# Optimization experiments

Hardware: AMD Instinct MI355X
Metric: run time of the kernel (lower is better)

Reference implementation:

```python
import jax, jax.numpy as jnp
import numpy as np

B, S, D = 1, 2048, 1024
NH, NKV, HD = 16, 4, 64
N_REP = NH // NKV


def _rope_tables(seq_len, half_dim, base=10000.0):
    inv_freq = 1.0 / (base ** (np.arange(0, half_dim, dtype=np.float32) / half_dim))
    t = np.arange(seq_len, dtype=np.float32)
    freqs = np.outer(t, inv_freq)  # (S, HD//2)
    return jnp.asarray(np.cos(freqs)), jnp.asarray(np.sin(freqs))


def setup_inputs() -> dict:
    key = jax.random.key(0)
    ks = jax.random.split(key, 5)
    x = jax.random.normal(ks[0], (B, S, D), dtype=jnp.float32)
    rope_cos, rope_sin = _rope_tables(S, HD // 2)
    sd = 1.0 / np.sqrt(D)
    Wq = jax.random.normal(ks[1], (D, NH * HD), dtype=jnp.float32) * sd
    Wk = jax.random.normal(ks[2], (D, NKV * HD), dtype=jnp.float32) * sd
    Wv = jax.random.normal(ks[3], (D, NKV * HD), dtype=jnp.float32) * sd
    Wo = jax.random.normal(ks[4], (NH * HD, D), dtype=jnp.float32) * sd
    return {"x": x, "rope_cos": rope_cos, "rope_sin": rope_sin,
            "Wq": Wq, "Wk": Wk, "Wv": Wv, "Wo": Wo}


def _apply_rope(t, cos, sin):
    # t: (B, H, S, HD); cos/sin: (S, HD//2). Rotate-half convention.
    t1, t2 = jnp.split(t, 2, axis=-1)
    c = cos[None, None, :, :]
    s = sin[None, None, :, :]
    return jnp.concatenate([t1 * c - t2 * s, t2 * c + t1 * s], axis=-1)


def reference(x, rope_cos, rope_sin, Wq, Wk, Wv, Wo):
    b, s, _ = x.shape
    # projections -> (B, H, S, HD)
    q = (x @ Wq).reshape(b, s, NH, HD).transpose(0, 2, 1, 3)
    k = (x @ Wk).reshape(b, s, NKV, HD).transpose(0, 2, 1, 3)
    v = (x @ Wv).reshape(b, s, NKV, HD).transpose(0, 2, 1, 3)
    q = _apply_rope(q, rope_cos, rope_sin)
    k = _apply_rope(k, rope_cos, rope_sin)
    # GQA expansion (repeat_interleave on head axis)
    k = jnp.repeat(k, N_REP, axis=1)
    v = jnp.repeat(v, N_REP, axis=1)
    scale = HD ** -0.5
    scores = jnp.einsum('bhqd,bhkd->bhqk', q, k) * scale
    causal = jnp.tril(jnp.ones((s, s), dtype=bool))
    scores = jnp.where(causal[None, None], scores, jnp.float32(-jnp.inf))
    attn = jax.nn.softmax(scores, axis=-1)
    out = jnp.einsum('bhqk,bhkd->bhqd', attn, v)  # (B, H, S, HD)
    out = out.transpose(0, 2, 1, 3).reshape(b, s, NH * HD)
    return out @ Wo
```

## Files before the change

kernel.cpp:

```cpp
#include <hip/hip_runtime.h>

typedef unsigned short ushort_t;
typedef __attribute__((ext_vector_type(8))) short short8;
typedef __attribute__((ext_vector_type(4))) float f32x4;
typedef __attribute__((ext_vector_type(4))) unsigned short ushort4v;
typedef __attribute__((ext_vector_type(8))) unsigned short ushort8v;

#define S_LEN 2048
#define D_MODEL 1024
#define NH 16
#define NKV 4
#define HD 64

__device__ __forceinline__ ushort_t f2bf(float f) {
    unsigned u = __float_as_uint(f);
    u += 0x7fffu + ((u >> 16) & 1u);
    return (ushort_t)(u >> 16);
}

__device__ __forceinline__ void cp16(void* lds, const void* g) {
    __builtin_amdgcn_global_load_lds(
        (__attribute__((address_space(1))) void*)g,
        (__attribute__((address_space(3))) void*)lds, 16, 0, 0);
}

__global__ __launch_bounds__(256) void prep_kernel(
    const float* __restrict__ x, ushort_t* __restrict__ xb,
    const float* __restrict__ Wq, const float* __restrict__ Wk,
    const float* __restrict__ Wv, const float* __restrict__ Wo,
    ushort_t* __restrict__ WqT, ushort_t* __restrict__ WkT,
    ushort_t* __restrict__ WvT, ushort_t* __restrict__ WoT)
{
    const int t = threadIdx.x;
    if (blockIdx.z == 4) {
        const int b  = blockIdx.y * 16 + blockIdx.x;
        const int i0 = (b * 256 + t) * 4;
        #pragma unroll
        for (int rep = 0; rep < 8; ++rep) {
            const int i = i0 + rep * 262144;
            float4 v = *(const float4*)(x + i);
            ushort4v o = { f2bf(v.x), f2bf(v.y), f2bf(v.z), f2bf(v.w) };
            *(ushort4v*)(xb + i) = o;
        }
        return;
    }
    __shared__ ushort_t T[64 * 72];
    const float* W; ushort_t* WT; int N;
    switch (blockIdx.z) {
        case 0:  W = Wq; WT = WqT; N = 1024; break;
        case 1:  W = Wk; WT = WkT; N = 256;  break;
        case 2:  W = Wv; WT = WvT; N = 256;  break;
        default: W = Wo; WT = WoT; N = 1024; break;
    }
    const int n0 = blockIdx.y * 64;
    if (n0 >= N) return;
    const int k0 = blockIdx.x * 64;
    const int kr = t >> 4, nc = (t & 15) * 4;
    #pragma unroll
    for (int p = 0; p < 4; ++p) {
        const int k = kr + p * 16;
        float4 v = *(const float4*)(W + (size_t)(k0 + k) * N + n0 + nc);
        T[(nc + 0) * 72 + k] = f2bf(v.x);
        T[(nc + 1) * 72 + k] = f2bf(v.y);
        T[(nc + 2) * 72 + k] = f2bf(v.z);
        T[(nc + 3) * 72 + k] = f2bf(v.w);
    }
    __syncthreads();
    const int n = t >> 2, seg = (t & 3) * 16;
    ushort8v a = *(ushort8v*)&T[n * 72 + seg];
    ushort8v b = *(ushort8v*)&T[n * 72 + seg + 8];
    *(ushort8v*)(WT + (size_t)(n0 + n) * 1024 + k0 + seg)     = a;
    *(ushort8v*)(WT + (size_t)(n0 + n) * 1024 + k0 + seg + 8) = b;
}

__global__ __launch_bounds__(256, 2) void gemm_qkv_mfma(
    const ushort_t* __restrict__ xb, const ushort_t* __restrict__ WqT,
    const ushort_t* __restrict__ WkT, const ushort_t* __restrict__ WvT,
    const float* __restrict__ rc, const float* __restrict__ rs,
    ushort_t* __restrict__ Qb, ushort_t* __restrict__ Kb,
    ushort_t* __restrict__ Vtb)
{
    __shared__ ushort_t As[4][64 * 64];
    __shared__ ushort_t Bs[4][64 * 64];

    const int t = threadIdx.x;
    const int lane = t & 63, wave = t >> 6;
    const int wr = wave >> 1, wc = wave & 1;
    const int quad = lane >> 4, l15 = lane & 15;
    const int lq = lane >> 3, lr = lane & 7;
    const int swz_st = (lr ^ lq) * 8;
    const int l7 = l15 & 7;
    const int fsw0 = (quad ^ l7) * 8;
    const int fsw1 = ((quad + 4) ^ l7) * 8;

    const int m0 = blockIdx.x * 64;
    const int cy = blockIdx.y;

    const ushort_t* WT; int nloc;
    if (cy < 16)      { WT = WqT; nloc = cy * 64; }
    else if (cy < 20) { WT = WkT; nloc = (cy - 16) * 64; }
    else              { WT = WvT; nloc = (cy - 20) * 64; }

    f32x4 acc[2][2];
    #pragma unroll
    for (int i = 0; i < 2; ++i)
        #pragma unroll
        for (int j = 0; j < 2; ++j) acc[i][j] = (f32x4)0.f;

    auto stage = [&](int buf, int k0) {
        #pragma unroll
        for (int i = 0; i < 2; ++i) {
            const int r = wave * 16 + i * 8 + lq;
            cp16(&As[buf][(wave * 16 + i * 8) * 64],
                 xb + (size_t)(m0 + r) * 1024 + k0 + swz_st);
            cp16(&Bs[buf][(wave * 16 + i * 8) * 64],
                 WT + (size_t)(nloc + r) * 1024 + k0 + swz_st);
        }
    };

    auto compute = [&](int cur) {
        const ushort_t* Ac = &As[cur][0];
        const ushort_t* Bc = &Bs[cur][0];
        #pragma unroll
        for (int h = 0; h < 2; ++h) {
            const int fsw = h ? fsw1 : fsw0;
            short8 av[2], bv[2];
            #pragma unroll
            for (int i = 0; i < 2; ++i)
                av[i] = *(const short8*)&Ac[(wr * 32 + i * 16 + l15) * 64 + fsw];
            #pragma unroll
            for (int j = 0; j < 2; ++j)
                bv[j] = *(const short8*)&Bc[(wc * 16 + j * 32 + l15) * 64 + fsw];
            #pragma unroll
            for (int i = 0; i < 2; ++i)
                #pragma unroll
                for (int j = 0; j < 2; ++j)
                    acc[i][j] = __builtin_amdgcn_mfma_f32_16x16x32_bf16(
                        av[i], bv[j], acc[i][j], 0, 0, 0);
        }
    };

    stage(0, 0);
    stage(1, 64);
    stage(2, 128);

    for (int kk = 0; kk < 14; ++kk) {
        asm volatile("s_waitcnt vmcnt(8)" ::: "memory");
        __builtin_amdgcn_s_barrier();
        __builtin_amdgcn_sched_barrier(0);
        if (kk < 13) stage((kk + 3) & 3, (kk + 3) * 64);
        compute(kk & 3);
    }
    asm volatile("s_waitcnt vmcnt(4)" ::: "memory");
    __builtin_amdgcn_s_barrier();
    __builtin_amdgcn_sched_barrier(0);
    compute(2);
    asm volatile("s_waitcnt vmcnt(0)" ::: "memory");
    __builtin_amdgcn_s_barrier();
    __builtin_amdgcn_sched_barrier(0);
    compute(3);

    if (cy < 20) {
        ushort_t* dst = (cy < 16) ? Qb : Kb;
        const int h = (cy < 16) ? cy : (cy - 16);
        const int d = wc * 16 + l15;
        #pragma unroll
        for (int i = 0; i < 2; ++i) {
            #pragma unroll
            for (int reg = 0; reg < 4; ++reg) {
                const int s = m0 + wr * 32 + i * 16 + quad * 4 + reg;
                const float c  = rc[s * 32 + d];
                const float sn = rs[s * 32 + d];
                const float v1 = acc[i][0][reg];
                const float v2 = acc[i][1][reg];
                dst[((size_t)h * S_LEN + s) * HD + d]      = f2bf(v1 * c - v2 * sn);
                dst[((size_t)h * S_LEN + s) * HD + d + 32] = f2bf(v2 * c + v1 * sn);
            }
        }
    } else {
        const int vh = cy - 20;
        #pragma unroll
        for (int i = 0; i < 2; ++i) {
            const int s0 = m0 + wr * 32 + i * 16 + quad * 4;
            #pragma unroll
            for (int j = 0; j < 2; ++j) {
                const int d = wc * 16 + j * 32 + l15;
                ushort4v o = { f2bf(acc[i][j][0]), f2bf(acc[i][j][1]),
                               f2bf(acc[i][j][2]), f2bf(acc[i][j][3]) };
                *(ushort4v*)&Vtb[((size_t)vh * HD + d) * S_LEN + s0] = o;
            }
        }
    }
}

__global__ __launch_bounds__(256, 2) void attn_mfma(
    const ushort_t* __restrict__ Qb, const ushort_t* __restrict__ Kb,
    const ushort_t* __restrict__ Vtb, ushort_t* __restrict__ attnb)
{
    __shared__ ushort_t Ks[2][2][64 * 64];
    __shared__ ushort_t Vs[2][2][64 * 64];
    __shared__ ushort_t Ps[4][16 * 72];

    const int t = threadIdx.x;
    const int lane = t & 63, wave = t >> 6;
    const int quad = lane >> 4, l15 = lane & 15;
    const int lq = lane >> 3, lr = lane & 7;
    const int swz_st = (lr ^ lq) * 8;
    const int l7 = l15 & 7;
    const int fsw0 = (quad ^ l7) * 8;
    const int fsw1 = ((quad + 4) ^ l7) * 8;

    const int h  = blockIdx.x;
    const int y  = blockIdx.y;
    const int qt = (y < 16) ? y : 47 - y;
    const int q0 = qt * 64;
    const int kvh = h >> 2;
    const int qrow0 = q0 + wave * 16;

    const ushort_t* Qg = Qb + ((size_t)h * S_LEN + qrow0) * HD;
    const ushort_t* Kg = Kb + (size_t)kvh * S_LEN * HD;
    const ushort_t* Vg = Vtb + (size_t)kvh * HD * S_LEN;

    short8 aq0 = *(const short8*)(Qg + (size_t)l15 * HD + quad * 8);
    short8 aq1 = *(const short8*)(Qg + (size_t)l15 * HD + 32 + quad * 8);

    float ps4[4] = {0.f, 0.f, 0.f, 0.f};
    f32x4 Oacc[4];
    #pragma unroll
    for (int jb = 0; jb < 4; ++jb) Oacc[jb] = (f32x4)0.f;

    const int nround = (qt + 2) >> 1;

    auto stage = [&](int buf, int kvbase) {
        #pragma unroll
        for (int u = 0; u < 2; ++u)
            #pragma unroll
            for (int i = 0; i < 2; ++i) {
                const int r = wave * 16 + i * 8 + lq;
                cp16(&Ks[buf][u][(wave * 16 + i * 8) * 64],
                     Kg + (size_t)(kvbase + u * 64 + r) * 64 + swz_st);
                cp16(&Vs[buf][u][(wave * 16 + i * 8) * 64],
                     Vg + (size_t)r * 2048 + kvbase + u * 64 + swz_st);
            }
    };

    stage(0, 0);
    __syncthreads();

    ushort_t* Pw = &Ps[wave][0];

    for (int round = 0; round < nround; ++round) {
        const int cur = round & 1;
        if (round + 1 < nround) stage(cur ^ 1, (round + 1) * 128);

        #pragma unroll
        for (int u = 0; u < 2; ++u) {
            const int kv0 = round * 128 + u * 64;
            if (kv0 > q0 + 63) break;
            const ushort_t* Kc = &Ks[cur][u][0];
            const ushort_t* Vc = &Vs[cur][u][0];

            f32x4 sv[4];
            #pragma unroll
            for (int jb = 0; jb < 4; ++jb) {
                short8 b0 = *(const short8*)&Kc[(jb * 16 + l15) * 64 + fsw0];
                short8 b1 = *(const short8*)&Kc[(jb * 16 + l15) * 64 + fsw1];
                f32x4 z = (f32x4)0.f;
                z = __builtin_amdgcn_mfma_f32_16x16x32_bf16(aq0, b0, z, 0, 0, 0);
                z = __builtin_amdgcn_mfma_f32_16x16x32_bf16(aq1, b1, z, 0, 0, 0);
                sv[jb] = z;
            }

            const bool diag = (kv0 == q0);
            #pragma unroll
            for (int jb = 0; jb < 4; ++jb) {
                const int col = kv0 + jb * 16 + l15;
                #pragma unroll
                for (int reg = 0; reg < 4; ++reg) {
                    float e = __expf(sv[jb][reg] * 0.125f);
                    if (diag && col > qrow0 + quad * 4 + reg) e = 0.f;
                    sv[jb][reg] = e;
                    ps4[reg] += e;
                }
            }

            #pragma unroll
            for (int jb = 0; jb < 4; ++jb)
                #pragma unroll
                for (int reg = 0; reg < 4; ++reg)
                    Pw[(quad * 4 + reg) * 72 + jb * 16 + l15] = f2bf(sv[jb][reg]);
            short8 p0 = *(const short8*)&Pw[l15 * 72 + quad * 8];
            short8 p1 = *(const short8*)&Pw[l15 * 72 + 32 + quad * 8];

            #pragma unroll
            for (int jb = 0; jb < 4; ++jb) {
                short8 v0 = *(const short8*)&Vc[(jb * 16 + l15) * 64 + fsw0];
                short8 v1 = *(const short8*)&Vc[(jb * 16 + l15) * 64 + fsw1];
                Oacc[jb] = __builtin_amdgcn_mfma_f32_16x16x32_bf16(p0, v0, Oacc[jb], 0, 0, 0);
                Oacc[jb] = __builtin_amdgcn_mfma_f32_16x16x32_bf16(p1, v1, Oacc[jb], 0, 0, 0);
            }
        }

        __syncthreads();
    }

    #pragma unroll
    for (int reg = 0; reg < 4; ++reg) {
        float l = ps4[reg];
        l += __shfl_xor(l, 1);
        l += __shfl_xor(l, 2);
        l += __shfl_xor(l, 4);
        l += __shfl_xor(l, 8);
        const float inv = 1.f / l;
        const int s = qrow0 + quad * 4 + reg;
        #pragma unroll
        for (int jb = 0; jb < 4; ++jb)
            attnb[(size_t)s * D_MODEL + h * HD + jb * 16 + l15] =
                f2bf(Oacc[jb][reg] * inv);
    }
}

__global__ __launch_bounds__(256, 2) void gemm_out_mfma(
    const ushort_t* __restrict__ Ab, const ushort_t* __restrict__ WoT,
    float* __restrict__ out)
{
    __shared__ ushort_t As[4][64 * 64];
    __shared__ ushort_t Bs[4][64 * 64];

    const int t = threadIdx.x;
    const int lane = t & 63, wave = t >> 6;
    const int wr = wave >> 1, wc = wave & 1;
    const int quad = lane >> 4, l15 = lane & 15;
    const int lq = lane >> 3, lr = lane & 7;
    const int swz_st = (lr ^ lq) * 8;
    const int l7 = l15 & 7;
    const int fsw0 = (quad ^ l7) * 8;
    const int fsw1 = ((quad + 4) ^ l7) * 8;

    const int m0 = blockIdx.x * 64;
    const int n0 = blockIdx.y * 64;

    f32x4 acc[2][2];
    #pragma unroll
    for (int i = 0; i < 2; ++i)
        #pragma unroll
        for (int j = 0; j < 2; ++j) acc[i][j] = (f32x4)0.f;

    auto stage = [&](int buf, int k0) {
        #pragma unroll
        for (int i = 0; i < 2; ++i) {
            const int r = wave * 16 + i * 8 + lq;
            cp16(&As[buf][(wave * 16 + i * 8) * 64],
                 Ab + (size_t)(m0 + r) * 1024 + k0 + swz_st);
            cp16(&Bs[buf][(wave * 16 + i * 8) * 64],
                 WoT + (size_t)(n0 + r) * 1024 + k0 + swz_st);
        }
    };

    auto compute = [&](int cur) {
        const ushort_t* Ac = &As[cur][0];
        const ushort_t* Bc = &Bs[cur][0];
        #pragma unroll
        for (int h = 0; h < 2; ++h) {
            const int fsw = h ? fsw1 : fsw0;
            short8 av[2], bv[2];
            #pragma unroll
            for (int i = 0; i < 2; ++i)
                av[i] = *(const short8*)&Ac[(wr * 32 + i * 16 + l15) * 64 + fsw];
            #pragma unroll
            for (int j = 0; j < 2; ++j)
                bv[j] = *(const short8*)&Bc[(wc * 32 + j * 16 + l15) * 64 + fsw];
            #pragma unroll
            for (int i = 0; i < 2; ++i)
                #pragma unroll
                for (int j = 0; j < 2; ++j)
                    acc[i][j] = __builtin_amdgcn_mfma_f32_16x16x32_bf16(
                        av[i], bv[j], acc[i][j], 0, 0, 0);
        }
    };

    stage(0, 0);
    stage(1, 64);
    stage(2, 128);

    for (int kk = 0; kk < 14; ++kk) {
        asm volatile("s_waitcnt vmcnt(8)" ::: "memory");
        __builtin_amdgcn_s_barrier();
        __builtin_amdgcn_sched_barrier(0);
        if (kk < 13) stage((kk + 3) & 3, (kk + 3) * 64);
        compute(kk & 3);
    }
    asm volatile("s_waitcnt vmcnt(4)" ::: "memory");
    __builtin_amdgcn_s_barrier();
    __builtin_amdgcn_sched_barrier(0);
    compute(2);
    asm volatile("s_waitcnt vmcnt(0)" ::: "memory");
    __builtin_amdgcn_s_barrier();
    __builtin_amdgcn_sched_barrier(0);
    compute(3);

    #pragma unroll
    for (int i = 0; i < 2; ++i)
        #pragma unroll
        for (int reg = 0; reg < 4; ++reg) {
            const int s = m0 + wr * 32 + i * 16 + quad * 4 + reg;
            #pragma unroll
            for (int j = 0; j < 2; ++j)
                out[(size_t)s * D_MODEL + n0 + wc * 32 + j * 16 + l15] = acc[i][j][reg];
        }
}

extern "C" void kernel_launch(void* const* d_in, const int* in_sizes, int n_in,
                              void* d_out, int out_size, void* d_ws, size_t ws_size,
                              hipStream_t stream)
{
    const float* x  = (const float*)d_in[0];
    const float* rc = (const float*)d_in[1];
    const float* rs = (const float*)d_in[2];
    const float* Wq = (const float*)d_in[3];
    const float* Wk = (const float*)d_in[4];
    const float* Wv = (const float*)d_in[5];
    const float* Wo = (const float*)d_in[6];
    float* out = (float*)d_out;

    ushort_t* xb   = (ushort_t*)d_ws;
    ushort_t* WqT  = xb   + (size_t)2048 * 1024;
    ushort_t* WkT  = WqT  + (size_t)1024 * 1024;
    ushort_t* WvT  = WkT  + (size_t)256 * 1024;
    ushort_t* WoT  = WvT  + (size_t)256 * 1024;
    ushort_t* Qb   = WoT  + (size_t)1024 * 1024;
    ushort_t* Kb   = Qb   + (size_t)NH * S_LEN * HD;
    ushort_t* Vtb  = Kb   + (size_t)NKV * S_LEN * HD;
    ushort_t* attnb= Vtb  + (size_t)NKV * HD * S_LEN;

    prep_kernel<<<dim3(16, 16, 5), 256, 0, stream>>>(x, xb, Wq, Wk, Wv, Wo,
                                                     WqT, WkT, WvT, WoT);
    gemm_qkv_mfma<<<dim3(32, 24), 256, 0, stream>>>(xb, WqT, WkT, WvT,
                                                    rc, rs, Qb, Kb, Vtb);
    attn_mfma<<<dim3(NH, 32), 256, 0, stream>>>(Qb, Kb, Vtb, attnb);
    gemm_out_mfma<<<dim3(32, 16), 256, 0, stream>>>(attnb, WoT, out);
}
```

Before: 140.5 us.

## Replace double-buffered 128-key rounds with 4-slot 64-key prefetch pipeline in attention

The attention kernel used to stage K/V in 128-key rounds with double buffering and a full __syncthreads per round. It now stages 64-key tiles into a 4-slot ring, prefetching three tiles ahead. Each step waits with explicit s_waitcnt vmcnt counts before a raw s_barrier. The aim is to hide global-to-LDS latency better and avoid loading a wasted half-round past the diagonal. The hand-written vmcnt counts must match the number of outstanding loads exactly, and there is still one barrier per 64-key tile.

```diff
diff --git a/kernel.cpp b/kernel.cpp
--- a/kernel.cpp
+++ b/kernel.cpp
@@ -197,8 +197,8 @@
     const ushort_t* __restrict__ Qb, const ushort_t* __restrict__ Kb,
     const ushort_t* __restrict__ Vtb, ushort_t* __restrict__ attnb)
 {
-    __shared__ ushort_t Ks[2][2][64 * 64];
-    __shared__ ushort_t Vs[2][2][64 * 64];
+    __shared__ ushort_t Ks[4][64 * 64];
+    __shared__ ushort_t Vs[4][64 * 64];
     __shared__ ushort_t Ps[4][16 * 72];
 
     const int t = threadIdx.x;
@@ -229,79 +229,79 @@
     #pragma unroll
     for (int jb = 0; jb < 4; ++jb) Oacc[jb] = (f32x4)0.f;
 
-    const int nround = (qt + 2) >> 1;
-
-    auto stage = [&](int buf, int kvbase) {
-        #pragma unroll
-        for (int u = 0; u < 2; ++u)
-            #pragma unroll
-            for (int i = 0; i < 2; ++i) {
-                const int r = wave * 16 + i * 8 + lq;
-                cp16(&Ks[buf][u][(wave * 16 + i * 8) * 64],
-                     Kg + (size_t)(kvbase + u * 64 + r) * 64 + swz_st);
-                cp16(&Vs[buf][u][(wave * 16 + i * 8) * 64],
-                     Vg + (size_t)r * 2048 + kvbase + u * 64 + swz_st);
+    const int nsub = qt + 1;
+
+    auto stage64 = [&](int s) {
+        const int kv0 = s * 64;
+        ushort_t* Kd = &Ks[s & 3][0];
+        ushort_t* Vd = &Vs[s & 3][0];
+        #pragma unroll
+        for (int i = 0; i < 2; ++i) {
+            const int rr = wave * 16 + i * 8;
+            const int r = rr + lq;
+            cp16(&Kd[rr * 64], Kg + (size_t)(kv0 + r) * 64 + swz_st);
+            cp16(&Vd[rr * 64], Vg + (size_t)r * 2048 + kv0 + swz_st);
+        }
+    };
+
+    stage64(0);
+    if (nsub > 1) stage64(1);
+    if (nsub > 2) stage64(2);
+
+    ushort_t* Pw = &Ps[wave][0];
+
+    for (int s = 0; s < nsub; ++s) {
+        const int rem = nsub - 1 - s;
+        if (rem >= 2)      asm volatile("s_waitcnt vmcnt(8)" ::: "memory");
+        else if (rem == 1) asm volatile("s_waitcnt vmcnt(4)" ::: "memory");
+        else               asm volatile("s_waitcnt vmcnt(0)" ::: "memory");
+        __builtin_amdgcn_s_barrier();
+        __builtin_amdgcn_sched_barrier(0);
+        if (s + 3 < nsub) stage64(s + 3);
+
+        const int kv0 = s * 64;
+        const ushort_t* Kc = &Ks[s & 3][0];
+        const ushort_t* Vc = &Vs[s & 3][0];
+
+        f32x4 sv[4];
+        #pragma unroll
+        for (int jb = 0; jb < 4; ++jb) {
+            short8 b0 = *(const short8*)&Kc[(jb * 16 + l15) * 64 + fsw0];
+            short8 b1 = *(const short8*)&Kc[(jb * 16 + l15) * 64 + fsw1];
+            f32x4 z = (f32x4)0.f;
+            z = __builtin_amdgcn_mfma_f32_16x16x32_bf16(aq0, b0, z, 0, 0, 0);
+            z = __builtin_amdgcn_mfma_f32_16x16x32_bf16(aq1, b1, z, 0, 0, 0);
+            sv[jb] = z;
+        }
+
+        const bool diag = (kv0 == q0);
+        #pragma unroll
+        for (int jb = 0; jb < 4; ++jb) {
+            const int col = kv0 + jb * 16 + l15;
+            #pragma unroll
+            for (int reg = 0; reg < 4; ++reg) {
+                float e = __expf(sv[jb][reg] * 0.125f);
+                if (diag && col > qrow0 + quad * 4 + reg) e = 0.f;
+                sv[jb][reg] = e;
+                ps4[reg] += e;
             }
-    };
-
-    stage(0, 0);
-    __syncthreads();
-
-    ushort_t* Pw = &Ps[wave][0];
-
-    for (int round = 0; round < nround; ++round) {
-        const int cur = round & 1;
-        if (round + 1 < nround) stage(cur ^ 1, (round + 1) * 128);
-
-        #pragma unroll
-        for (int u = 0; u < 2; ++u) {
-            const int kv0 = round * 128 + u * 64;
-            if (kv0 > q0 + 63) break;
-            const ushort_t* Kc = &Ks[cur][u][0];
-            const ushort_t* Vc = &Vs[cur][u][0];
-
-            f32x4 sv[4];
-            #pragma unroll
-            for (int jb = 0; jb < 4; ++jb) {
-                short8 b0 = *(const short8*)&Kc[(jb * 16 + l15) * 64 + fsw0];
-                short8 b1 = *(const short8*)&Kc[(jb * 16 + l15) * 64 + fsw1];
-                f32x4 z = (f32x4)0.f;
-                z = __builtin_amdgcn_mfma_f32_16x16x32_bf16(aq0, b0, z, 0, 0, 0);
-                z = __builtin_amdgcn_mfma_f32_16x16x32_bf16(aq1, b1, z, 0, 0, 0);
-                sv[jb] = z;
-            }
-
-            const bool diag = (kv0 == q0);
-            #pragma unroll
-            for (int jb = 0; jb < 4; ++jb) {
-                const int col = kv0 + jb * 16 + l15;
-                #pragma unroll
-                for (int reg = 0; reg < 4; ++reg) {
-                    float e = __expf(sv[jb][reg] * 0.125f);
-                    if (diag && col > qrow0 + quad * 4 + reg) e = 0.f;
-                    sv[jb][reg] = e;
-                    ps4[reg] += e;
-                }
-            }
-
-            #pragma unroll
-            for (int jb = 0; jb < 4; ++jb)
-                #pragma unroll
-                for (int reg = 0; reg < 4; ++reg)
-                    Pw[(quad * 4 + reg) * 72 + jb * 16 + l15] = f2bf(sv[jb][reg]);
-            short8 p0 = *(const short8*)&Pw[l15 * 72 + quad * 8];
-            short8 p1 = *(const short8*)&Pw[l15 * 72 + 32 + quad * 8];
-
-            #pragma unroll
-            for (int jb = 0; jb < 4; ++jb) {
-                short8 v0 = *(const short8*)&Vc[(jb * 16 + l15) * 64 + fsw0];
-                short8 v1 = *(const short8*)&Vc[(jb * 16 + l15) * 64 + fsw1];
-                Oacc[jb] = __builtin_amdgcn_mfma_f32_16x16x32_bf16(p0, v0, Oacc[jb], 0, 0, 0);
-                Oacc[jb] = __builtin_amdgcn_mfma_f32_16x16x32_bf16(p1, v1, Oacc[jb], 0, 0, 0);
-            }
-        }
-
-        __syncthreads();
+        }
+
+        #pragma unroll
+        for (int jb = 0; jb < 4; ++jb)
+            #pragma unroll
+            for (int reg = 0; reg < 4; ++reg)
+                Pw[(quad * 4 + reg) * 72 + jb * 16 + l15] = f2bf(sv[jb][reg]);
+        short8 p0 = *(const short8*)&Pw[l15 * 72 + quad * 8];
+        short8 p1 = *(const short8*)&Pw[l15 * 72 + 32 + quad * 8];
+
+        #pragma unroll
+        for (int jb = 0; jb < 4; ++jb) {
+            short8 v0 = *(const short8*)&Vc[(jb * 16 + l15) * 64 + fsw0];
+            short8 v1 = *(const short8*)&Vc[(jb * 16 + l15) * 64 + fsw1];
+            Oacc[jb] = __builtin_amdgcn_mfma_f32_16x16x32_bf16(p0, v0, Oacc[jb], 0, 0, 0);
+            Oacc[jb] = __builtin_amdgcn_mfma_f32_16x16x32_bf16(p1, v1, Oacc[jb], 0, 0, 0);
+        }
     }
 
     #pragma unroll
```

Result: slower. 146.3 us (+4.1%).

## Split attention tile into 2x2 wave grid over query and KV halves

Applied to the files above, without the earlier changes.

Each wave now covers 32 query rows and half of each 64-key chunk, not 16 rows over all keys. K and V fragments loaded from LDS are reused across two query sub-tiles, which halves LDS fragment reads per MFMA. Waves whose KV half lies fully above the diagonal skip that chunk. The two KV-half partial outputs and row sums are combined through LDS at the end, which adds an extra barrier and a reduction step.

```diff
diff --git a/kernel.cpp b/kernel.cpp
--- a/kernel.cpp
+++ b/kernel.cpp
@@ -199,7 +199,7 @@
 {
     __shared__ ushort_t Ks[2][2][64 * 64];
     __shared__ ushort_t Vs[2][2][64 * 64];
-    __shared__ ushort_t Ps[4][16 * 72];
+    __shared__ ushort_t Ps[4][32 * 40];
 
     const int t = threadIdx.x;
     const int lane = t & 63, wave = t >> 6;
@@ -207,27 +207,44 @@
     const int lq = lane >> 3, lr = lane & 7;
     const int swz_st = (lr ^ lq) * 8;
     const int l7 = l15 & 7;
-    const int fsw0 = (quad ^ l7) * 8;
-    const int fsw1 = ((quad + 4) ^ l7) * 8;
+
+    const int qh  = wave >> 1;
+    const int kvh = wave & 1;
+    const int kvL0 = kvh * 32;
+
+    const int fswK0 = (quad ^ l7) * 8;
+    const int fswK1 = ((quad + 4) ^ l7) * 8;
+    const int fswV  = (((kvh << 2) + quad) ^ l7) * 8;
 
     const int h  = blockIdx.x;
     const int y  = blockIdx.y;
     const int qt = (y < 16) ? y : 47 - y;
     const int q0 = qt * 64;
-    const int kvh = h >> 2;
-    const int qrow0 = q0 + wave * 16;
+    const int kvhead = h >> 2;
+    const int qrow0 = q0 + qh * 32;
 
     const ushort_t* Qg = Qb + ((size_t)h * S_LEN + qrow0) * HD;
-    const ushort_t* Kg = Kb + (size_t)kvh * S_LEN * HD;
-    const ushort_t* Vg = Vtb + (size_t)kvh * HD * S_LEN;
-
-    short8 aq0 = *(const short8*)(Qg + (size_t)l15 * HD + quad * 8);
-    short8 aq1 = *(const short8*)(Qg + (size_t)l15 * HD + 32 + quad * 8);
-
-    float ps4[4] = {0.f, 0.f, 0.f, 0.f};
-    f32x4 Oacc[4];
-    #pragma unroll
-    for (int jb = 0; jb < 4; ++jb) Oacc[jb] = (f32x4)0.f;
+    const ushort_t* Kg = Kb + (size_t)kvhead * S_LEN * HD;
+    const ushort_t* Vg = Vtb + (size_t)kvhead * HD * S_LEN;
+
+    short8 aq[2][2];
+    #pragma unroll
+    for (int mq = 0; mq < 2; ++mq)
+        #pragma unroll
+        for (int kh = 0; kh < 2; ++kh)
+            aq[mq][kh] = *(const short8*)(Qg + (size_t)(mq * 16 + l15) * HD
+                                          + kh * 32 + quad * 8);
+
+    float ps[2][4];
+    #pragma unroll
+    for (int mq = 0; mq < 2; ++mq)
+        #pragma unroll
+        for (int r = 0; r < 4; ++r) ps[mq][r] = 0.f;
+    f32x4 Oacc[2][4];
+    #pragma unroll
+    for (int mq = 0; mq < 2; ++mq)
+        #pragma unroll
+        for (int jb = 0; jb < 4; ++jb) Oacc[mq][jb] = (f32x4)0.f;
 
     const int nround = (qt + 2) >> 1;
 
@@ -257,66 +274,112 @@
         for (int u = 0; u < 2; ++u) {
             const int kv0 = round * 128 + u * 64;
             if (kv0 > q0 + 63) break;
+            const bool diag = (kv0 == q0);
+            if (diag && kvL0 > qh * 32 + 31) continue;
             const ushort_t* Kc = &Ks[cur][u][0];
             const ushort_t* Vc = &Vs[cur][u][0];
 
-            f32x4 sv[4];
+            short8 kb[2][2];
+            #pragma unroll
+            for (int jbl = 0; jbl < 2; ++jbl) {
+                kb[jbl][0] = *(const short8*)&Kc[(kvL0 + jbl * 16 + l15) * 64 + fswK0];
+                kb[jbl][1] = *(const short8*)&Kc[(kvL0 + jbl * 16 + l15) * 64 + fswK1];
+            }
+
+            f32x4 sv[2][2];
+            #pragma unroll
+            for (int mq = 0; mq < 2; ++mq)
+                #pragma unroll
+                for (int jbl = 0; jbl < 2; ++jbl) {
+                    f32x4 z = (f32x4)0.f;
+                    z = __builtin_amdgcn_mfma_f32_16x16x32_bf16(aq[mq][0], kb[jbl][0], z, 0, 0, 0);
+                    z = __builtin_amdgcn_mfma_f32_16x16x32_bf16(aq[mq][1], kb[jbl][1], z, 0, 0, 0);
+                    sv[mq][jbl] = z;
+                }
+
+            #pragma unroll
+            for (int mq = 0; mq < 2; ++mq)
+                #pragma unroll
+                for (int jbl = 0; jbl < 2; ++jbl) {
+                    const int colg = kv0 + kvL0 + jbl * 16 + l15;
+                    #pragma unroll
+                    for (int reg = 0; reg < 4; ++reg) {
+                        float e = __expf(sv[mq][jbl][reg] * 0.125f);
+                        const int qg = qrow0 + mq * 16 + quad * 4 + reg;
+                        if (diag && colg > qg) e = 0.f;
+                        sv[mq][jbl][reg] = e;
+                        ps[mq][reg] += e;
+                    }
+                }
+
+            #pragma unroll
+            for (int mq = 0; mq < 2; ++mq)
+                #pragma unroll
+                for (int jbl = 0; jbl < 2; ++jbl)
+                    #pragma unroll
+                    for (int reg = 0; reg < 4; ++reg)
+                        Pw[(mq * 16 + quad * 4 + reg) * 40 + jbl * 16 + l15] =
+                            f2bf(sv[mq][jbl][reg]);
+            short8 pa[2];
+            #pragma unroll
+            for (int mq = 0; mq < 2; ++mq)
+                pa[mq] = *(const short8*)&Pw[(mq * 16 + l15) * 40 + quad * 8];
+
             #pragma unroll
             for (int jb = 0; jb < 4; ++jb) {
-                short8 b0 = *(const short8*)&Kc[(jb * 16 + l15) * 64 + fsw0];
-                short8 b1 = *(const short8*)&Kc[(jb * 16 + l15) * 64 + fsw1];
-                f32x4 z = (f32x4)0.f;
-                z = __builtin_amdgcn_mfma_f32_16x16x32_bf16(aq0, b0, z, 0, 0, 0);
-                z = __builtin_amdgcn_mfma_f32_16x16x32_bf16(aq1, b1, z, 0, 0, 0);
-                sv[jb] = z;
-            }
-
-            const bool diag = (kv0 == q0);
-            #pragma unroll
-            for (int jb = 0; jb < 4; ++jb) {
-                const int col = kv0 + jb * 16 + l15;
-                #pragma unroll
-                for (int reg = 0; reg < 4; ++reg) {
-                    float e = __expf(sv[jb][reg] * 0.125f);
-                    if (diag && col > qrow0 + quad * 4 + reg) e = 0.f;
-                    sv[jb][reg] = e;
-                    ps4[reg] += e;
+                short8 vb = *(const short8*)&Vc[(jb * 16 + l15) * 64 + fswV];
+                Oacc[0][jb] = __builtin_amdgcn_mfma_f32_16x16x32_bf16(pa[0], vb, Oacc[0][jb], 0, 0, 0);
+                Oacc[1][jb] = __builtin_amdgcn_mfma_f32_16x16x32_bf16(pa[1], vb, Oacc[1][jb], 0, 0, 0);
+            }
+        }
+
+        __syncthreads();
+    }
+
+    #pragma unroll
+    for (int mq = 0; mq < 2; ++mq)
+        #pragma unroll
+        for (int reg = 0; reg < 4; ++reg) {
+            float l = ps[mq][reg];
+            l += __shfl_xor(l, 1);
+            l += __shfl_xor(l, 2);
+            l += __shfl_xor(l, 4);
+            l += __shfl_xor(l, 8);
+            ps[mq][reg] = l;
+        }
+
+    float* Rbuf = (float*)&Ks[0][0][0];
+    if (kvh == 1) {
+        #pragma unroll
+        for (int mq = 0; mq < 2; ++mq)
+            #pragma unroll
+            for (int reg = 0; reg < 4; ++reg) {
+                const int row = mq * 16 + quad * 4 + reg;
+                #pragma unroll
+                for (int jb = 0; jb < 4; ++jb)
+                    Rbuf[qh * 2176 + row * 68 + jb * 16 + l15] = Oacc[mq][jb][reg];
+                if (l15 == 0)
+                    Rbuf[qh * 2176 + row * 68 + 64] = ps[mq][reg];
+            }
+    }
+    __syncthreads();
+    if (kvh == 0) {
+        #pragma unroll
+        for (int mq = 0; mq < 2; ++mq)
+            #pragma unroll
+            for (int reg = 0; reg < 4; ++reg) {
+                const int row = mq * 16 + quad * 4 + reg;
+                const float ltot = ps[mq][reg] + Rbuf[qh * 2176 + row * 68 + 64];
+                const float inv = 1.f / ltot;
+                const int sq = qrow0 + row;
+                #pragma unroll
+                for (int jb = 0; jb < 4; ++jb) {
+                    const float o = Oacc[mq][jb][reg]
+                                  + Rbuf[qh * 2176 + row * 68 + jb * 16 + l15];
+                    attnb[(size_t)sq * D_MODEL + h * HD + jb * 16 + l15] =
+                        f2bf(o * inv);
                 }
             }
-
-            #pragma unroll
-            for (int jb = 0; jb < 4; ++jb)
-                #pragma unroll
-                for (int reg = 0; reg < 4; ++reg)
-                    Pw[(quad * 4 + reg) * 72 + jb * 16 + l15] = f2bf(sv[jb][reg]);
-            short8 p0 = *(const short8*)&Pw[l15 * 72 + quad * 8];
-            short8 p1 = *(const short8*)&Pw[l15 * 72 + 32 + quad * 8];
-
-            #pragma unroll
-            for (int jb = 0; jb < 4; ++jb) {
-                short8 v0 = *(const short8*)&Vc[(jb * 16 + l15) * 64 + fsw0];
-                short8 v1 = *(const short8*)&Vc[(jb * 16 + l15) * 64 + fsw1];
-                Oacc[jb] = __builtin_amdgcn_mfma_f32_16x16x32_bf16(p0, v0, Oacc[jb], 0, 0, 0);
-                Oacc[jb] = __builtin_amdgcn_mfma_f32_16x16x32_bf16(p1, v1, Oacc[jb], 0, 0, 0);
-            }
-        }
-
-        __syncthreads();
-    }
-
-    #pragma unroll
-    for (int reg = 0; reg < 4; ++reg) {
-        float l = ps4[reg];
-        l += __shfl_xor(l, 1);
-        l += __shfl_xor(l, 2);
-        l += __shfl_xor(l, 4);
-        l += __shfl_xor(l, 8);
-        const float inv = 1.f / l;
-        const int s = qrow0 + quad * 4 + reg;
-        #pragma unroll
-        for (int jb = 0; jb < 4; ++jb)
-            attnb[(size_t)s * D_MODEL + h * HD + jb * 16 + l15] =
-                f2bf(Oacc[jb][reg] * inv);
     }
 }
 
```

Measured after the change: 140.7 us. About the same (+0.1%).

## Halve attention query tile to 32 rows with 2-wave blocks and more blocks

Applied to the files above, without the earlier changes.

The attention kernel now uses 128-thread blocks, each covering 32 query rows, and launches twice as many blocks, with a new balanced tile-ordering map. The K/V staging no longer double-buffers: each round loads two 64-key subtiles, synchronises, then computes. The smaller tiles waste less work on the causal diagonal and give finer load balancing. In exchange, each K/V tile is reloaded by more blocks, and global loads no longer overlap with compute.

```diff
diff --git a/kernel.cpp b/kernel.cpp
--- a/kernel.cpp
+++ b/kernel.cpp
@@ -193,13 +193,13 @@
     }
 }
 
-__global__ __launch_bounds__(256, 2) void attn_mfma(
+__global__ __launch_bounds__(128, 2) void attn_mfma(
     const ushort_t* __restrict__ Qb, const ushort_t* __restrict__ Kb,
     const ushort_t* __restrict__ Vtb, ushort_t* __restrict__ attnb)
 {
-    __shared__ ushort_t Ks[2][2][64 * 64];
-    __shared__ ushort_t Vs[2][2][64 * 64];
-    __shared__ ushort_t Ps[4][16 * 72];
+    __shared__ ushort_t Ks[2][64 * 64];
+    __shared__ ushort_t Vs[2][64 * 64];
+    __shared__ ushort_t Ps[2][16 * 72];
 
     const int t = threadIdx.x;
     const int lane = t & 63, wave = t >> 6;
@@ -210,10 +210,10 @@
     const int fsw0 = (quad ^ l7) * 8;
     const int fsw1 = ((quad + 4) ^ l7) * 8;
 
-    const int h  = blockIdx.x;
-    const int y  = blockIdx.y;
-    const int qt = (y < 16) ? y : 47 - y;
-    const int q0 = qt * 64;
+    const int h = blockIdx.x;
+    const int z = blockIdx.y;
+    const int T = (z & 16) ? ((z < 32) ? 47 - z : 111 - z) : z;
+    const int q0 = T * 32;
     const int kvh = h >> 2;
     const int qrow0 = q0 + wave * 16;
 
@@ -229,49 +229,49 @@
     #pragma unroll
     for (int jb = 0; jb < 4; ++jb) Oacc[jb] = (f32x4)0.f;
 
-    const int nround = (qt + 2) >> 1;
-
-    auto stage = [&](int buf, int kvbase) {
-        #pragma unroll
-        for (int u = 0; u < 2; ++u)
-            #pragma unroll
-            for (int i = 0; i < 2; ++i) {
-                const int r = wave * 16 + i * 8 + lq;
-                cp16(&Ks[buf][u][(wave * 16 + i * 8) * 64],
-                     Kg + (size_t)(kvbase + u * 64 + r) * 64 + swz_st);
-                cp16(&Vs[buf][u][(wave * 16 + i * 8) * 64],
-                     Vg + (size_t)r * 2048 + kvbase + u * 64 + swz_st);
-            }
+    const int nsub = (q0 + 31) / 64 + 1;
+    const int nround = (nsub + 1) >> 1;
+
+    auto stage = [&](int u, int sidx) {
+        const int kv0 = sidx * 64;
+        #pragma unroll
+        for (int i = 0; i < 4; ++i) {
+            const int rr = wave * 32 + i * 8;
+            const int r = rr + lq;
+            cp16(&Ks[u][rr * 64], Kg + (size_t)(kv0 + r) * 64 + swz_st);
+            cp16(&Vs[u][rr * 64], Vg + (size_t)r * 2048 + kv0 + swz_st);
+        }
     };
 
-    stage(0, 0);
-    __syncthreads();
-
     ushort_t* Pw = &Ps[wave][0];
 
     for (int round = 0; round < nround; ++round) {
-        const int cur = round & 1;
-        if (round + 1 < nround) stage(cur ^ 1, (round + 1) * 128);
+        const int s0 = round * 2;
+        if (round) __syncthreads();
+        stage(0, s0);
+        if (s0 + 1 < nsub) stage(1, s0 + 1);
+        __syncthreads();
 
         #pragma unroll
         for (int u = 0; u < 2; ++u) {
-            const int kv0 = round * 128 + u * 64;
-            if (kv0 > q0 + 63) break;
-            const ushort_t* Kc = &Ks[cur][u][0];
-            const ushort_t* Vc = &Vs[cur][u][0];
+            const int sidx = s0 + u;
+            if (sidx >= nsub) break;
+            const int kv0 = sidx * 64;
+            const bool diag = (sidx == nsub - 1);
+            const ushort_t* Kc = &Ks[u][0];
+            const ushort_t* Vc = &Vs[u][0];
 
             f32x4 sv[4];
             #pragma unroll
             for (int jb = 0; jb < 4; ++jb) {
                 short8 b0 = *(const short8*)&Kc[(jb * 16 + l15) * 64 + fsw0];
                 short8 b1 = *(const short8*)&Kc[(jb * 16 + l15) * 64 + fsw1];
-                f32x4 z = (f32x4)0.f;
-                z = __builtin_amdgcn_mfma_f32_16x16x32_bf16(aq0, b0, z, 0, 0, 0);
-                z = __builtin_amdgcn_mfma_f32_16x16x32_bf16(aq1, b1, z, 0, 0, 0);
-                sv[jb] = z;
+                f32x4 zv = (f32x4)0.f;
+                zv = __builtin_amdgcn_mfma_f32_16x16x32_bf16(aq0, b0, zv, 0, 0, 0);
+                zv = __builtin_amdgcn_mfma_f32_16x16x32_bf16(aq1, b1, zv, 0, 0, 0);
+                sv[jb] = zv;
             }
 
-            const bool diag = (kv0 == q0);
             #pragma unroll
             for (int jb = 0; jb < 4; ++jb) {
                 const int col = kv0 + jb * 16 + l15;
@@ -300,8 +300,6 @@
                 Oacc[jb] = __builtin_amdgcn_mfma_f32_16x16x32_bf16(p1, v1, Oacc[jb], 0, 0, 0);
             }
         }
-
-        __syncthreads();
     }
 
     #pragma unroll
@@ -312,10 +310,10 @@
         l += __shfl_xor(l, 4);
         l += __shfl_xor(l, 8);
         const float inv = 1.f / l;
-        const int s = qrow0 + quad * 4 + reg;
+        const int srow = qrow0 + quad * 4 + reg;
         #pragma unroll
         for (int jb = 0; jb < 4; ++jb)
-            attnb[(size_t)s * D_MODEL + h * HD + jb * 16 + l15] =
+            attnb[(size_t)srow * D_MODEL + h * HD + jb * 16 + l15] =
                 f2bf(Oacc[jb][reg] * inv);
     }
 }
@@ -437,6 +435,6 @@
                                                      WqT, WkT, WvT, WoT);
     gemm_qkv_mfma<<<dim3(32, 24), 256, 0, stream>>>(xb, WqT, WkT, WvT,
                                                     rc, rs, Qb, Kb, Vtb);
-    attn_mfma<<<dim3(NH, 32), 256, 0, stream>>>(Qb, Kb, Vtb, attnb);
+    attn_mfma<<<dim3(NH, 64), 128, 0, stream>>>(Qb, Kb, Vtb, attnb);
     gemm_out_mfma<<<dim3(32, 16), 256, 0, stream>>>(attnb, WoT, out);
 }
```

Result: slower. 143.4 us (+2.1%).
